# Kernel optimization log

Hardware: AMD Instinct MI355X
Metric: run time of the kernel (lower is better)

## Reference

```python
import jax, jax.numpy as jnp
import numpy as np

MAT_MODE = ((0, 1), (0, 2), (1, 2))
VEC_MODE = (2, 1, 0)
DENSITY_SHIFT = -10.0
DISTANCE_SCALE = 25.0


def grid_sample_2d(img, coords):
    # img: [C, H, W]; coords: [N, 2] in [-1, 1], (x indexes W, y indexes H);
    # bilinear, align_corners=True (matches F.grid_sample in the source).
    C, H, W = img.shape
    x = (coords[:, 0] + 1.0) * 0.5 * (W - 1)
    y = (coords[:, 1] + 1.0) * 0.5 * (H - 1)
    x0 = jnp.floor(x)
    y0 = jnp.floor(y)
    wx = x - x0
    wy = y - y0
    x0i = jnp.clip(x0.astype(jnp.int32), 0, W - 1)
    x1i = jnp.clip(x0i + 1, 0, W - 1)
    y0i = jnp.clip(y0.astype(jnp.int32), 0, H - 1)
    y1i = jnp.clip(y0i + 1, 0, H - 1)
    v00 = img[:, y0i, x0i]
    v01 = img[:, y0i, x1i]
    v10 = img[:, y1i, x0i]
    v11 = img[:, y1i, x1i]
    return (v00 * (1 - wx) * (1 - wy) + v01 * wx * (1 - wy)
            + v10 * (1 - wx) * wy + v11 * wx * wy)  # [C, N]


def line_sample_1d(line, t):
    # line: [C, L]; t: [N] in [-1, 1]. Equivalent to the source's grid_sample on a
    # [1, C, L, 1] tensor with coords (0, t): the width dim (size 1) collapses.
    C, L = line.shape
    y = (t + 1.0) * 0.5 * (L - 1)
    y0 = jnp.floor(y)
    wy = y - y0
    y0i = jnp.clip(y0.astype(jnp.int32), 0, L - 1)
    y1i = jnp.clip(y0i + 1, 0, L - 1)
    return line[:, y0i] * (1 - wy) + line[:, y1i] * wy  # [C, N]


def tensorf_features(planes, lines, xyz):
    # planes: [3, C, H, W]; lines: [3, C, L]; xyz: [N, 3] normalized coords.
    # fusion_two='concat' then fusion_one='multiply' == per-plane multiply, concat.
    feats = []
    for i in range(3):
        a, b = MAT_MODE[i]
        pc = jnp.stack([xyz[:, a], xyz[:, b]], axis=-1)  # [N, 2]
        pf = grid_sample_2d(planes[i], pc)               # [C, N]
        lf = line_sample_1d(lines[i], xyz[:, VEC_MODE[i]])  # [C, N]
        feats.append(pf * lf)
    return jnp.concatenate(feats, axis=0)  # [3C, N]


def raw2alpha(sigma, dist):
    # sigma, dist: [Nr, Ns]
    alpha = 1.0 - jnp.exp(-sigma * dist)
    T = jnp.cumprod(jnp.concatenate(
        [jnp.ones((alpha.shape[0], 1), alpha.dtype), 1.0 - alpha + 1e-10], axis=-1), axis=-1)
    weights = alpha * T[:, :-1]
    return alpha, weights, T[:, -1:]


def setup_inputs() -> dict:
    key = jax.random.key(0)
    ks = jax.random.split(key, 10)
    Nr, Ns, G = 4096, 256, 300
    aabb = jnp.array([[-1.5, -1.5, -1.5], [1.5, 1.5, 1.5]], jnp.float32)
    xyz_sampled = jax.random.uniform(ks[0], (Nr, Ns, 3), jnp.float32,
                                     minval=-1.5, maxval=1.5)
    vd = jax.random.normal(ks[1], (Nr, 3), jnp.float32)
    viewdirs = vd / jnp.linalg.norm(vd, axis=-1, keepdims=True)
    near, far = 2.0, 6.0
    t = jnp.linspace(0.0, 1.0, Ns, dtype=jnp.float32)
    z_vals = near * (1.0 - t) + far * t
    z_vals = jnp.broadcast_to(z_vals, (Nr, Ns)) + \
        jax.random.uniform(ks[2], (Nr, Ns), jnp.float32) * ((far - near) / Ns)
    z_vals = jnp.sort(z_vals, axis=-1)
    s = 0.1  # init_scale
    return {
        'xyz_sampled': xyz_sampled,
        'viewdirs': viewdirs,
        'z_vals': z_vals,
        'density_planes': s * jax.random.normal(ks[3], (3, 8, G, G), jnp.float32),
        'density_lines': s * jax.random.normal(ks[4], (3, 8, G), jnp.float32),
        'app_planes': s * jax.random.normal(ks[5], (3, 24, G, G), jnp.float32),
        'app_lines': s * jax.random.normal(ks[6], (3, 24, G), jnp.float32),
        'density_basis_w': jnp.ones((1, 24), jnp.float32),  # source inits to 1/density_dim
        'app_basis_w': s * jax.random.normal(ks[7], (3, 72), jnp.float32),
        'aabb': aabb,
    }


def reference(xyz_sampled, viewdirs, z_vals, density_planes, density_lines,
              app_planes, app_lines, density_basis_w, app_basis_w, aabb):
    Nr, Ns, _ = xyz_sampled.shape
    # normalize_coord: map aabb -> [-1, 1]
    inv_size = 2.0 / (aabb[1] - aabb[0])
    xyz = ((xyz_sampled - aabb[0]) * inv_size - 1.0).reshape(-1, 3)  # [N, 3]

    dfeat = tensorf_features(density_planes, density_lines, xyz)      # [24, N]
    sigma_feat = (density_basis_w @ dfeat).reshape(Nr, Ns)            # basis_mat
    sigma = jax.nn.softplus(sigma_feat + DENSITY_SHIFT)               # fea2denseAct

    # ray-marching distances
    dists = z_vals[:, 1:] - z_vals[:, :-1]
    dists = jnp.concatenate([dists, dists[:, -1:]], axis=-1)
    alpha, weights, bg_T = raw2alpha(sigma, dists * DISTANCE_SCALE)

    # appearance branch: RGBRender is identity on the 3-dim basis output
    afeat = tensorf_features(app_planes, app_lines, xyz)              # [72, N]
    rgb = (app_basis_w @ afeat).T.reshape(Nr, Ns, 3)

    rgb_map = jnp.sum(weights[..., None] * rgb, axis=1)               # [Nr, 3]
    return rgb_map
```

## Files before the change

### kernel.cpp

```cpp
#include <hip/hip_runtime.h>
#include <math.h>

#define G  300
#define NS 256
#define NR 4096
#define CT 32

typedef _Float16 half16_t;
typedef _Float16 h8 __attribute__((ext_vector_type(8)));
typedef float f4v __attribute__((ext_vector_type(4)));

__global__ __launch_bounds__(256) void prep_planes(
    const float* __restrict__ dp, const float* __restrict__ ap,
    half16_t* __restrict__ out)
{
  int t = blockIdx.x * blockDim.x + threadIdx.x;
  if (t >= 3 * G * G * 4) return;
  int m   = t & 3;
  int tex = t >> 2;
  int x  = tex % G;
  int yi = tex / G;
  int y  = yi % G;
  int i  = yi / G;
  const size_t GG = (size_t)G * G;
  const float* p = (m == 0) ? (dp + (size_t)(i * 8) * GG + (size_t)y * G + x)
                            : (ap + (size_t)(i * 24 + (m - 1) * 8) * GG + (size_t)y * G + x);
  h8 v;
#pragma unroll
  for (int c = 0; c < 8; ++c) v[c] = (half16_t)p[c * GG];
  *(h8*)(out + (size_t)tex * CT + m * 8) = v;
}

__global__ __launch_bounds__(256) void prep_lines(
    const float* __restrict__ dl, const float* __restrict__ al,
    half16_t* __restrict__ out)
{
  int t = blockIdx.x * blockDim.x + threadIdx.x;
  if (t >= 3 * G * 4) return;
  int m   = t & 3;
  int tex = t >> 2;
  int p = tex % G;
  int i = tex / G;
  h8 v;
#pragma unroll
  for (int c = 0; c < 8; ++c)
    v[c] = (m == 0) ? (half16_t)dl[(i * 8 + c) * G + p]
                    : (half16_t)al[(i * 24 + (m - 1) * 8 + c) * G + p];
  *(h8*)(out + (size_t)tex * CT + m * 8) = v;
}

#define ITER 4

__global__ __launch_bounds__(256) void tensorf_gather(
    const float* __restrict__ xyz,
    const half16_t* __restrict__ planes, const half16_t* __restrict__ lns,
    const float* __restrict__ dbw, const float* __restrict__ abw,
    const float* __restrict__ aabb, f4v* __restrict__ feat)
{
  const int lane = threadIdx.x & 63;
  const int wv   = threadIdx.x >> 6;
  const int q    = lane >> 2;
  const int r    = lane & 3;
  const int waveId = (blockIdx.x << 2) + wv;

  float W[3][24];
  if (r == 0) {
#pragma unroll
    for (int m = 0; m < 24; ++m) { W[0][m] = dbw[m]; W[1][m] = 0.f; W[2][m] = 0.f; }
  } else {
#pragma unroll
    for (int j = 0; j < 3; ++j)
#pragma unroll
      for (int i = 0; i < 3; ++i)
#pragma unroll
        for (int k = 0; k < 8; ++k)
          W[j][i * 8 + k] = abw[j * 72 + i * 24 + (r - 1) * 8 + k];
  }

  const float a0x = aabb[0], a0y = aabb[1], a0z = aabb[2];
  const float ivx = 2.f / (aabb[3] - aabb[0]);
  const float ivy = 2.f / (aabb[4] - aabb[1]);
  const float ivz = 2.f / (aabb[5] - aabb[2]);

  const int MA[3] = {0, 0, 1};
  const int MB[3] = {1, 2, 2};
  const int MV[3] = {2, 1, 0};
  const int ro = r * 8;

#pragma unroll 1
  for (int it = 0; it < ITER; ++it) {
    int s = (waveId * ITER + it) * 16 + q;
    const float* xp = xyz + (size_t)s * 3;
    float px = __builtin_nontemporal_load(xp + 0);
    float py = __builtin_nontemporal_load(xp + 1);
    float pz = __builtin_nontemporal_load(xp + 2);
    float g[3];
    g[0] = (px - a0x) * ivx - 1.f;
    g[1] = (py - a0y) * ivy - 1.f;
    g[2] = (pz - a0z) * ivz - 1.f;

    float acc0 = 0.f, acc1 = 0.f, acc2 = 0.f;
#pragma unroll
    for (int i = 0; i < 3; ++i) {
      float fx = (g[MA[i]] + 1.f) * (0.5f * (G - 1));
      float fy = (g[MB[i]] + 1.f) * (0.5f * (G - 1));
      float ft = (g[MV[i]] + 1.f) * (0.5f * (G - 1));
      float x0f = floorf(fx), y0f = floorf(fy), t0f = floorf(ft);
      float wx = fx - x0f, wy = fy - y0f, wt = ft - t0f;
      int x0 = min(max((int)x0f, 0), G - 1);
      int y0 = min(max((int)y0f, 0), G - 1);
      int t0 = min(max((int)t0f, 0), G - 1);
      int x1 = min(x0 + 1, G - 1);
      int y1 = min(y0 + 1, G - 1);
      int t1 = min(t0 + 1, G - 1);

      const half16_t* pb = planes + (size_t)i * G * G * CT;
      h8 t00 = *(const h8*)(pb + ((size_t)(y0 * G + x0)) * CT + ro);
      h8 t01 = *(const h8*)(pb + ((size_t)(y0 * G + x1)) * CT + ro);
      h8 t10 = *(const h8*)(pb + ((size_t)(y1 * G + x0)) * CT + ro);
      h8 t11 = *(const h8*)(pb + ((size_t)(y1 * G + x1)) * CT + ro);
      const half16_t* lb = lns + (size_t)i * G * CT + ro;
      h8 l0 = *(const h8*)(lb + (size_t)t0 * CT);
      h8 l1 = *(const h8*)(lb + (size_t)t1 * CT);

      float w00 = (1.f - wx) * (1.f - wy), w01 = wx * (1.f - wy);
      float w10 = (1.f - wx) * wy,         w11 = wx * wy;
      float wl0 = 1.f - wt;
#pragma unroll
      for (int k = 0; k < 8; ++k) {
        float pf = (float)t00[k] * w00 + (float)t01[k] * w01
                 + (float)t10[k] * w10 + (float)t11[k] * w11;
        float lf = (float)l0[k] * wl0 + (float)l1[k] * wt;
        float f  = pf * lf;
        acc0 += W[0][i * 8 + k] * f;
        acc1 += W[1][i * 8 + k] * f;
        acc2 += W[2][i * 8 + k] * f;
      }
    }
    f4v v;
    v.x = (r == 0) ? acc0 : 0.f;
    v.y = (r == 0) ? 0.f : acc0;
    v.z = (r == 0) ? 0.f : acc1;
    v.w = (r == 0) ? 0.f : acc2;
#pragma unroll
    for (int m = 1; m <= 2; m <<= 1) {
      v.x += __shfl_xor(v.x, m);
      v.y += __shfl_xor(v.y, m);
      v.z += __shfl_xor(v.z, m);
      v.w += __shfl_xor(v.w, m);
    }
    if (r == 0) __builtin_nontemporal_store(v, feat + s);
  }
}

__global__ __launch_bounds__(256) void tensorf_scan(
    const float* __restrict__ zv, const f4v* __restrict__ feat,
    float* __restrict__ out)
{
  const int wv   = threadIdx.x >> 6;
  const int lane = threadIdx.x & 63;
  const int ray  = (blockIdx.x << 2) + wv;

  const f4v* zp = (const f4v*)(zv + (size_t)ray * NS + lane * 4);
  f4v z4 = __builtin_nontemporal_load(zp);
  float znext = __shfl_down(z4.x, 1);
  float d[4];
  d[0] = z4.y - z4.x;
  d[1] = z4.z - z4.y;
  d[2] = z4.w - z4.z;
  d[3] = (lane == 63) ? d[2] : (znext - z4.w);

  f4v c[4];
  float al[4];
  float tl = 1.f;
#pragma unroll
  for (int j = 0; j < 4; ++j) {
    c[j] = __builtin_nontemporal_load(feat + (size_t)ray * NS + lane * 4 + j);
    float vs = c[j].x - 10.0f;
    float sp = (vs > 0.f) ? (vs + log1pf(expf(-vs))) : log1pf(expf(vs));
    al[j] = 1.f - expf(-sp * (d[j] * 25.0f));
    tl *= (1.f - al[j] + 1e-10f);
  }
  float incl = tl;
#pragma unroll
  for (int off = 1; off < 64; off <<= 1) {
    float p = __shfl_up(incl, off);
    if (lane >= off) incl *= p;
  }
  float T = __shfl_up(incl, 1);
  if (lane == 0) T = 1.f;

  float ar = 0.f, ag = 0.f, ab = 0.f;
#pragma unroll
  for (int j = 0; j < 4; ++j) {
    float w = al[j] * T;
    ar += w * c[j].y;
    ag += w * c[j].z;
    ab += w * c[j].w;
    T *= (1.f - al[j] + 1e-10f);
  }
#pragma unroll
  for (int off = 32; off > 0; off >>= 1) {
    ar += __shfl_down(ar, off);
    ag += __shfl_down(ag, off);
    ab += __shfl_down(ab, off);
  }
  if (lane == 0) {
    out[ray * 3 + 0] = ar;
    out[ray * 3 + 1] = ag;
    out[ray * 3 + 2] = ab;
  }
}

extern "C" void kernel_launch(void* const* d_in, const int* in_sizes, int n_in,
                              void* d_out, int out_size, void* d_ws, size_t ws_size,
                              hipStream_t stream)
{
  const float* xyz  = (const float*)d_in[0];
  const float* zv   = (const float*)d_in[2];
  const float* dp   = (const float*)d_in[3];
  const float* dl   = (const float*)d_in[4];
  const float* ap   = (const float*)d_in[5];
  const float* al   = (const float*)d_in[6];
  const float* dbw  = (const float*)d_in[7];
  const float* abw  = (const float*)d_in[8];
  const float* aabb = (const float*)d_in[9];
  float* out = (float*)d_out;

  half16_t* planes16 = (half16_t*)d_ws;
  half16_t* lines16  = planes16 + (size_t)3 * G * G * CT;
  f4v*      feat     = (f4v*)(lines16 + (size_t)3 * G * CT);

  hipLaunchKernelGGL(prep_planes, dim3((3 * G * G * 4 + 255) / 256), dim3(256), 0, stream,
                     dp, ap, planes16);
  hipLaunchKernelGGL(prep_lines, dim3((3 * G * 4 + 255) / 256), dim3(256), 0, stream,
                     dl, al, lines16);
  hipLaunchKernelGGL(tensorf_gather, dim3(NR * NS / (16 * ITER * 4)), dim3(256), 0, stream,
                     xyz, planes16, lines16, dbw, abw, aabb, feat);
  hipLaunchKernelGGL(tensorf_scan, dim3(NR / 4), dim3(256), 0, stream,
                     zv, feat, out);
}
```

Before: 246.8 us.

## Counting-sort samples into spatial cells before the texture gather

Adds a histogram, a single-block prefix scan and a scatter pass that counting-sort the 1M sample points into a 16x16x16 spatial grid. The gather kernel then reads points in sorted order, with blocks interleaved across the grid, and writes features back by original index. The aim is better cache locality for the random fp16 plane and line lookups. The cost is extra passes over the sample data, contended atomics in the histogram and scatter, and scattered feature stores.

```diff
diff --git a/kernel.cpp b/kernel.cpp
--- a/kernel.cpp
+++ b/kernel.cpp
@@ -5,30 +5,58 @@
 #define NS 256
 #define NR 4096
 #define CT 32
+#define NB 16
+#define NCELL (NB*NB*NB)
+#define NSAMP (NR*NS)
 
 typedef _Float16 half16_t;
 typedef _Float16 h8 __attribute__((ext_vector_type(8)));
 typedef float f4v __attribute__((ext_vector_type(4)));
 
-__global__ __launch_bounds__(256) void prep_planes(
+__device__ __forceinline__ int cell_of(float px, float py, float pz,
+                                       float a0x, float a0y, float a0z,
+                                       float ivx, float ivy, float ivz)
+{
+  float gx = (px - a0x) * ivx - 1.f;
+  float gy = (py - a0y) * ivy - 1.f;
+  float gz = (pz - a0z) * ivz - 1.f;
+  int bx = min(max((int)((gx + 1.f) * (0.5f * NB)), 0), NB - 1);
+  int by = min(max((int)((gy + 1.f) * (0.5f * NB)), 0), NB - 1);
+  int bz = min(max((int)((gz + 1.f) * (0.5f * NB)), 0), NB - 1);
+  return (bz * NB + by) * NB + bx;
+}
+
+__global__ __launch_bounds__(256) void prep_planes_hist(
     const float* __restrict__ dp, const float* __restrict__ ap,
-    half16_t* __restrict__ out)
+    const float* __restrict__ xyz, const float* __restrict__ aabb,
+    half16_t* __restrict__ out, int* __restrict__ hist)
 {
   int t = blockIdx.x * blockDim.x + threadIdx.x;
-  if (t >= 3 * G * G * 4) return;
-  int m   = t & 3;
-  int tex = t >> 2;
-  int x  = tex % G;
-  int yi = tex / G;
-  int y  = yi % G;
-  int i  = yi / G;
-  const size_t GG = (size_t)G * G;
-  const float* p = (m == 0) ? (dp + (size_t)(i * 8) * GG + (size_t)y * G + x)
-                            : (ap + (size_t)(i * 24 + (m - 1) * 8) * GG + (size_t)y * G + x);
-  h8 v;
-#pragma unroll
-  for (int c = 0; c < 8; ++c) v[c] = (half16_t)p[c * GG];
-  *(h8*)(out + (size_t)tex * CT + m * 8) = v;
+  if (t < 3 * G * G * 4) {
+    int m   = t & 3;
+    int tex = t >> 2;
+    int x  = tex % G;
+    int yi = tex / G;
+    int y  = yi % G;
+    int i  = yi / G;
+    const size_t GG = (size_t)G * G;
+    const float* p = (m == 0) ? (dp + (size_t)(i * 8) * GG + (size_t)y * G + x)
+                              : (ap + (size_t)(i * 24 + (m - 1) * 8) * GG + (size_t)y * G + x);
+    h8 v;
+#pragma unroll
+    for (int c = 0; c < 8; ++c) v[c] = (half16_t)p[c * GG];
+    *(h8*)(out + (size_t)tex * CT + m * 8) = v;
+  }
+  if (t < NSAMP) {
+    float px = xyz[(size_t)t * 3 + 0];
+    float py = xyz[(size_t)t * 3 + 1];
+    float pz = xyz[(size_t)t * 3 + 2];
+    float ivx = 2.f / (aabb[3] - aabb[0]);
+    float ivy = 2.f / (aabb[4] - aabb[1]);
+    float ivz = 2.f / (aabb[5] - aabb[2]);
+    int c = cell_of(px, py, pz, aabb[0], aabb[1], aabb[2], ivx, ivy, ivz);
+    atomicAdd(&hist[c], 1);
+  }
 }
 
 __global__ __launch_bounds__(256) void prep_lines(
@@ -49,10 +77,54 @@
   *(h8*)(out + (size_t)tex * CT + m * 8) = v;
 }
 
+__global__ __launch_bounds__(1024) void prefix4096(
+    const int* __restrict__ hist, int* __restrict__ offs)
+{
+  __shared__ int lds[1024];
+  int tid = threadIdx.x;
+  int4 h = ((const int4*)hist)[tid];
+  int s = h.x + h.y + h.z + h.w;
+  lds[tid] = s;
+  __syncthreads();
+#pragma unroll
+  for (int off = 1; off < 1024; off <<= 1) {
+    int u = 0;
+    if (tid >= off) u = lds[tid - off];
+    __syncthreads();
+    if (tid >= off) lds[tid] += u;
+    __syncthreads();
+  }
+  int excl = lds[tid] - s;
+  int4 o;
+  o.x = excl;
+  o.y = o.x + h.x;
+  o.z = o.y + h.y;
+  o.w = o.z + h.z;
+  ((int4*)offs)[tid] = o;
+}
+
+__global__ __launch_bounds__(256) void scatter_sorted(
+    const float* __restrict__ xyz, const float* __restrict__ aabb,
+    int* __restrict__ offs, f4v* __restrict__ sxyz)
+{
+  int t = blockIdx.x * blockDim.x + threadIdx.x;
+  if (t >= NSAMP) return;
+  float px = xyz[(size_t)t * 3 + 0];
+  float py = xyz[(size_t)t * 3 + 1];
+  float pz = xyz[(size_t)t * 3 + 2];
+  float ivx = 2.f / (aabb[3] - aabb[0]);
+  float ivy = 2.f / (aabb[4] - aabb[1]);
+  float ivz = 2.f / (aabb[5] - aabb[2]);
+  int c = cell_of(px, py, pz, aabb[0], aabb[1], aabb[2], ivx, ivy, ivz);
+  int pos = atomicAdd(&offs[c], 1);
+  f4v v = {px, py, pz, __int_as_float(t)};
+  __builtin_nontemporal_store(v, sxyz + pos);
+}
+
 #define ITER 4
 
 __global__ __launch_bounds__(256) void tensorf_gather(
-    const float* __restrict__ xyz,
+    const f4v* __restrict__ sxyz,
     const half16_t* __restrict__ planes, const half16_t* __restrict__ lns,
     const float* __restrict__ dbw, const float* __restrict__ abw,
     const float* __restrict__ aabb, f4v* __restrict__ feat)
@@ -61,7 +133,7 @@
   const int wv   = threadIdx.x >> 6;
   const int q    = lane >> 2;
   const int r    = lane & 3;
-  const int waveId = (blockIdx.x << 2) + wv;
+  const int cb   = (blockIdx.x & 7) * (gridDim.x >> 3) + (blockIdx.x >> 3);
 
   float W[3][24];
   if (r == 0) {
@@ -89,11 +161,10 @@
 
 #pragma unroll 1
   for (int it = 0; it < ITER; ++it) {
-    int s = (waveId * ITER + it) * 16 + q;
-    const float* xp = xyz + (size_t)s * 3;
-    float px = __builtin_nontemporal_load(xp + 0);
-    float py = __builtin_nontemporal_load(xp + 1);
-    float pz = __builtin_nontemporal_load(xp + 2);
+    int slot = (cb * 16 + wv * ITER + it) * 16 + q;
+    f4v sx = sxyz[slot];
+    float px = sx.x, py = sx.y, pz = sx.z;
+    int id = __float_as_int(sx.w);
     float g[3];
     g[0] = (px - a0x) * ivx - 1.f;
     g[1] = (py - a0y) * ivy - 1.f;
@@ -149,7 +220,7 @@
       v.z += __shfl_xor(v.z, m);
       v.w += __shfl_xor(v.w, m);
     }
-    if (r == 0) __builtin_nontemporal_store(v, feat + s);
+    if (r == 0) __builtin_nontemporal_store(v, feat + id);
   }
 }
 
@@ -227,16 +298,24 @@
   const float* aabb = (const float*)d_in[9];
   float* out = (float*)d_out;
 
-  half16_t* planes16 = (half16_t*)d_ws;
-  half16_t* lines16  = planes16 + (size_t)3 * G * G * CT;
-  f4v*      feat     = (f4v*)(lines16 + (size_t)3 * G * CT);
-
-  hipLaunchKernelGGL(prep_planes, dim3((3 * G * G * 4 + 255) / 256), dim3(256), 0, stream,
-                     dp, ap, planes16);
+  char* w = (char*)d_ws;
+  half16_t* planes16 = (half16_t*)w;                 w += (size_t)3 * G * G * CT * 2;
+  half16_t* lines16  = (half16_t*)w;                 w += (size_t)3 * G * CT * 2;
+  f4v*      feat     = (f4v*)w;                      w += (size_t)NSAMP * 16;
+  f4v*      sxyz     = (f4v*)w;                      w += (size_t)NSAMP * 16;
+  int*      hist     = (int*)w;                      w += (size_t)NCELL * 4;
+  int*      offs     = (int*)w;                      w += (size_t)NCELL * 4;
+
+  hipMemsetAsync(hist, 0, NCELL * sizeof(int), stream);
+  hipLaunchKernelGGL(prep_planes_hist, dim3((3 * G * G * 4 + 255) / 256), dim3(256), 0, stream,
+                     dp, ap, xyz, aabb, planes16, hist);
   hipLaunchKernelGGL(prep_lines, dim3((3 * G * 4 + 255) / 256), dim3(256), 0, stream,
                      dl, al, lines16);
-  hipLaunchKernelGGL(tensorf_gather, dim3(NR * NS / (16 * ITER * 4)), dim3(256), 0, stream,
-                     xyz, planes16, lines16, dbw, abw, aabb, feat);
+  hipLaunchKernelGGL(prefix4096, dim3(1), dim3(1024), 0, stream, hist, offs);
+  hipLaunchKernelGGL(scatter_sorted, dim3((NSAMP + 255) / 256), dim3(256), 0, stream,
+                     xyz, aabb, offs, sxyz);
+  hipLaunchKernelGGL(tensorf_gather, dim3(NSAMP / (16 * ITER * 4)), dim3(256), 0, stream,
+                     sxyz, planes16, lines16, dbw, abw, aabb, feat);
   hipLaunchKernelGGL(tensorf_scan, dim3(NR / 4), dim3(256), 0, stream,
                      zv, feat, out);
 }
```

New measurement: 361.0 us. +46.2%, slower.
